# Performance work log

Measured on AMD Instinct MI355X. Metric: run time of the kernel, lower is better.

Reference implementation:

```python
import jax, jax.numpy as jnp
import numpy as np
from jax import lax

B, T, N = 512, 512, 64  # batch, max_seq_len, num_tags


def setup_inputs() -> dict:
    key = jax.random.key(0)
    k1, k2, k3, k4 = jax.random.split(key, 4)
    inputs = jax.random.normal(k1, (B, T, N), dtype=jnp.float32)
    transition_params = jax.random.normal(k2, (N, N), dtype=jnp.float32)
    tag_indices = jax.random.randint(k3, (B, T), 0, N, dtype=jnp.int32)
    sequence_lengths = jax.random.randint(k4, (B,), 0, T, dtype=jnp.int32)
    return {
        "inputs": inputs,
        "transition_params": transition_params,
        "tag_indices": tag_indices,
        "sequence_lengths": sequence_lengths,
    }


def _crf_log_norm(inputs, transition_params, sequence_lengths):
    # inputs: [B, T, N]
    first = inputs[:, 0, :]                       # alpha after first token, [B, N]
    rest = jnp.transpose(inputs[:, 1:, :], (1, 0, 2))  # [T-1, B, N]

    def step(alpha, emit):
        # alpha: [B, N] -> broadcast-add transitions [N, N], logsumexp over prev tag
        new = emit + jax.nn.logsumexp(alpha[:, :, None] + transition_params[None], axis=1)
        return new, new

    _, alphas = lax.scan(step, first, rest)       # [T-1, B, N]
    all_alphas = jnp.concatenate([first[None], alphas], axis=0)  # [T, B, N]
    all_alphas = jnp.transpose(all_alphas, (1, 0, 2))            # [B, T, N]
    last_index = jnp.maximum(0, sequence_lengths - 1)            # [B]
    alpha_last = jnp.take_along_axis(all_alphas, last_index[:, None, None], axis=1)[:, 0, :]
    return jax.nn.logsumexp(alpha_last, axis=1)   # [B]


def _crf_sequence_score(inputs, tag_indices, sequence_lengths, transition_params):
    mask = (jnp.arange(T)[None, :] < sequence_lengths[:, None]).astype(inputs.dtype)  # [B, T]
    # unary: gather emission score of the gold tag at each position
    unary = jnp.take_along_axis(inputs, tag_indices[:, :, None], axis=2)[:, :, 0]      # [B, T]
    unary_scores = jnp.sum(unary * mask, axis=1)
    # binary: transition scores between consecutive gold tags
    binary = transition_params[tag_indices[:, :-1], tag_indices[:, 1:]]                # [B, T-1]
    binary_scores = jnp.sum(binary * mask[:, 1:], axis=1)
    return unary_scores + binary_scores


def reference(inputs, transition_params, tag_indices, sequence_lengths):
    tag_indices = tag_indices.astype(jnp.int32)
    sequence_lengths = sequence_lengths.astype(jnp.int32)
    sequence_scores = _crf_sequence_score(inputs, tag_indices, sequence_lengths, transition_params)
    log_norm = _crf_log_norm(inputs, transition_params, sequence_lengths)
    log_likelihood = sequence_scores - log_norm   # [B]
    return (log_likelihood, transition_params)
```

## Files before the change

kernel.cpp:

```cpp
#include <hip/hip_runtime.h>

#define BB 512
#define TT 512
#define NN 64

__device__ __forceinline__ float readlane_f(float v, int lane) {
    return __int_as_float(__builtin_amdgcn_readlane(__float_as_int(v), lane));
}


#define DOTG(g, Ev) \
    s0 = fmaf(readlane_f(p, 4 * (g) + 0), Ev.x, s0); \
    s1 = fmaf(readlane_f(p, 4 * (g) + 1), Ev.y, s1); \
    s2 = fmaf(readlane_f(p, 4 * (g) + 2), Ev.z, s2); \
    s3 = fmaf(readlane_f(p, 4 * (g) + 3), Ev.w, s3);

#define DOT64(p, sres) { \
    float s0 = readlane_f(p, 0) * E0.x; \
    float s1 = readlane_f(p, 1) * E0.y; \
    float s2 = readlane_f(p, 2) * E0.z; \
    float s3 = readlane_f(p, 3) * E0.w; \
    DOTG(1, E1)  DOTG(2, E2)  DOTG(3, E3) \
    DOTG(4, E4)  DOTG(5, E5)  DOTG(6, E6)  DOTG(7, E7) \
    DOTG(8, E8)  DOTG(9, E9)  DOTG(10, E10) DOTG(11, E11) \
    DOTG(12, E12) DOTG(13, E13) DOTG(14, E14) DOTG(15, E15) \
    sres = (s0 + s1) + (s2 + s3); \
}

__global__ __launch_bounds__(64, 1) void crf_kernel(
    const float* __restrict__ inputs,
    const float* __restrict__ trans,
    const int*   __restrict__ tags,
    const int*   __restrict__ lens,
    float*       __restrict__ out)
{
    const int b = blockIdx.x;
    const int j = threadIdx.x;

    if (b < 64) out[BB + b * 64 + j] = trans[b * 64 + j];

    const int L    = lens[b];
    const int last = (L - 1) > 0 ? (L - 1) : 0;

    const float* inb  = inputs + (size_t)b * TT * NN;
    const int*   tagb = tags + (size_t)b * TT;

    float sc = 0.f;
    #pragma unroll
    for (int k = 0; k < 8; ++k) {
        const int t  = k * 64 + j;
        const int tg = tagb[t];
        if (t < L) sc += inb[t * NN + tg];
        if (t + 1 < L) sc += trans[tg * NN + tagb[t + 1]];
    }
    #pragma unroll
    for (int x = 32; x >= 1; x >>= 1) sc += __shfl_xor(sc, x, 64);

    float4 E0, E1, E2, E3, E4, E5, E6, E7, E8, E9, E10, E11, E12, E13, E14, E15;
#define LDE(Ev, g) \
    Ev.x = __expf(trans[(4 * (g) + 0) * NN + j]); \
    Ev.y = __expf(trans[(4 * (g) + 1) * NN + j]); \
    Ev.z = __expf(trans[(4 * (g) + 2) * NN + j]); \
    Ev.w = __expf(trans[(4 * (g) + 3) * NN + j]);
    LDE(E0, 0)   LDE(E1, 1)   LDE(E2, 2)   LDE(E3, 3)
    LDE(E4, 4)   LDE(E5, 5)   LDE(E6, 6)   LDE(E7, 7)
    LDE(E8, 8)   LDE(E9, 9)   LDE(E10, 10) LDE(E11, 11)
    LDE(E12, 12) LDE(E13, 13) LDE(E14, 14) LDE(E15, 15)
#undef LDE

    float alpha = inb[j];

    float4 pA0, pA1, pA2, pA3, pB0, pB1, pB2, pB3;

#define LD(vec, comp, tt) { const int tc_ = (tt) <= last ? (tt) : last; \
                            vec.comp = inb[tc_ * NN + j]; }
#define LOADCHUNK(v0, v1, v2, v3, base) \
    LD(v0, x, (base) + 0)  LD(v0, y, (base) + 1)  LD(v0, z, (base) + 2)  LD(v0, w, (base) + 3)  \
    LD(v1, x, (base) + 4)  LD(v1, y, (base) + 5)  LD(v1, z, (base) + 6)  LD(v1, w, (base) + 7)  \
    LD(v2, x, (base) + 8)  LD(v2, y, (base) + 9)  LD(v2, z, (base) + 10) LD(v2, w, (base) + 11) \
    LD(v3, x, (base) + 12) LD(v3, y, (base) + 13) LD(v3, z, (base) + 14) LD(v3, w, (base) + 15)

#define STEP(tc_, EM) { \
    const float m = readlane_f(alpha, 0); \
    const float p = __expf(alpha - m); \
    float s; \
    DOT64(p, s) \
    if ((tc_) <= last) alpha = ((EM) + m) + __logf(s); \
}

    LOADCHUNK(pA0, pA1, pA2, pA3, 1)

    for (int t0 = 1; t0 <= last; t0 += 32) {
        LOADCHUNK(pB0, pB1, pB2, pB3, t0 + 16)
        STEP(t0 + 0,  pA0.x) STEP(t0 + 1,  pA0.y) STEP(t0 + 2,  pA0.z) STEP(t0 + 3,  pA0.w)
        STEP(t0 + 4,  pA1.x) STEP(t0 + 5,  pA1.y) STEP(t0 + 6,  pA1.z) STEP(t0 + 7,  pA1.w)
        STEP(t0 + 8,  pA2.x) STEP(t0 + 9,  pA2.y) STEP(t0 + 10, pA2.z) STEP(t0 + 11, pA2.w)
        STEP(t0 + 12, pA3.x) STEP(t0 + 13, pA3.y) STEP(t0 + 14, pA3.z) STEP(t0 + 15, pA3.w)
        LOADCHUNK(pA0, pA1, pA2, pA3, t0 + 32)
        STEP(t0 + 16, pB0.x) STEP(t0 + 17, pB0.y) STEP(t0 + 18, pB0.z) STEP(t0 + 19, pB0.w)
        STEP(t0 + 20, pB1.x) STEP(t0 + 21, pB1.y) STEP(t0 + 22, pB1.z) STEP(t0 + 23, pB1.w)
        STEP(t0 + 24, pB2.x) STEP(t0 + 25, pB2.y) STEP(t0 + 26, pB2.z) STEP(t0 + 27, pB2.w)
        STEP(t0 + 28, pB3.x) STEP(t0 + 29, pB3.y) STEP(t0 + 30, pB3.z) STEP(t0 + 31, pB3.w)
    }
#undef STEP
#undef LOADCHUNK
#undef LD

    float mm = alpha;
    #pragma unroll
    for (int x = 32; x >= 1; x >>= 1) mm = fmaxf(mm, __shfl_xor(mm, x, 64));
    float e = __expf(alpha - mm);
    #pragma unroll
    for (int x = 32; x >= 1; x >>= 1) e += __shfl_xor(e, x, 64);
    if (j == 0) out[b] = sc - (mm + __logf(e));
}

extern "C" void kernel_launch(void* const* d_in, const int* in_sizes, int n_in,
                              void* d_out, int out_size, void* d_ws, size_t ws_size,
                              hipStream_t stream) {
    const float* inputs = (const float*)d_in[0];
    const float* trans  = (const float*)d_in[1];
    const int*   tags   = (const int*)d_in[2];
    const int*   lens   = (const int*)d_in[3];
    float*       out    = (float*)d_out;

    crf_kernel<<<dim3(BB), dim3(64), 0, stream>>>(inputs, trans, tags, lens, out);
}
```

Baseline: 226.6 us.

## Interleave two batch recurrences per wavefront to overlap serial CRF step latency

Each wavefront now runs the forward recurrence for two batch elements (b and b+256) in lockstep, with half as many blocks launched. The goal is to hide the latency of the serial chain in each step (readlane, exp, 64-term dot, log) by giving the scheduler two independent chains to overlap. The max used for stabilisation is now read from the previous alpha instead of the current one, which takes the readlane off the critical path but loosens the guard against exp overflow. The transition exponentials are pinned in registers and the prefetch chunk shrinks to 4 steps per sequence; each pair now runs until the longer of its two sequences is done.

```diff
diff --git a/kernel.cpp b/kernel.cpp
--- a/kernel.cpp
+++ b/kernel.cpp
@@ -3,6 +3,7 @@
 #define BB 512
 #define TT 512
 #define NN 64
+#define NPAIR 256
 
 __device__ __forceinline__ float readlane_f(float v, int lane) {
     return __int_as_float(__builtin_amdgcn_readlane(__float_as_int(v), lane));
@@ -20,12 +21,25 @@
     float s1 = readlane_f(p, 1) * E0.y; \
     float s2 = readlane_f(p, 2) * E0.z; \
     float s3 = readlane_f(p, 3) * E0.w; \
-    DOTG(1, E1)  DOTG(2, E2)  DOTG(3, E3) \
-    DOTG(4, E4)  DOTG(5, E5)  DOTG(6, E6)  DOTG(7, E7) \
-    DOTG(8, E8)  DOTG(9, E9)  DOTG(10, E10) DOTG(11, E11) \
+    DOTG(1, E1)   DOTG(2, E2)   DOTG(3, E3) \
+    DOTG(4, E4)   DOTG(5, E5)   DOTG(6, E6)   DOTG(7, E7) \
+    DOTG(8, E8)   DOTG(9, E9)   DOTG(10, E10) DOTG(11, E11) \
     DOTG(12, E12) DOTG(13, E13) DOTG(14, E14) DOTG(15, E15) \
     sres = (s0 + s1) + (s2 + s3); \
 }
+
+#define STEP1(av, mv, EMv, tc_, lastv) { \
+    const float mu = mv; \
+    const float p  = __expf(av - mu); \
+    mv = readlane_f(av, 0);    \
+    float s; \
+    DOT64(p, s) \
+    if ((tc_) <= lastv) av = ((EMv) + mu) + __logf(s); \
+}
+
+#define DSTEP(r, EA, EB) \
+    STEP1(alpha0, m0, EA, t0 + (r), last0) \
+    STEP1(alpha1, m1, EB, t0 + (r), last1)
 
 __global__ __launch_bounds__(64, 1) void crf_kernel(
     const float* __restrict__ inputs,
@@ -39,22 +53,32 @@
 
     if (b < 64) out[BB + b * 64 + j] = trans[b * 64 + j];
 
-    const int L    = lens[b];
-    const int last = (L - 1) > 0 ? (L - 1) : 0;
+    const int L0 = lens[b];
+    const int L1 = lens[b + NPAIR];
+    const int last0 = (L0 - 1) > 0 ? (L0 - 1) : 0;
+    const int last1 = (L1 - 1) > 0 ? (L1 - 1) : 0;
+    const int lastmax = last0 > last1 ? last0 : last1;
 
-    const float* inb  = inputs + (size_t)b * TT * NN;
-    const int*   tagb = tags + (size_t)b * TT;
+    const float* inb0 = inputs + (size_t)b * TT * NN;
+    const float* inb1 = inputs + (size_t)(b + NPAIR) * TT * NN;
+    const int*   tagb0 = tags + (size_t)b * TT;
+    const int*   tagb1 = tags + (size_t)(b + NPAIR) * TT;
 
-    float sc = 0.f;
+    float sc0 = 0.f, sc1 = 0.f;
     #pragma unroll
     for (int k = 0; k < 8; ++k) {
-        const int t  = k * 64 + j;
-        const int tg = tagb[t];
-        if (t < L) sc += inb[t * NN + tg];
-        if (t + 1 < L) sc += trans[tg * NN + tagb[t + 1]];
+        const int t = k * 64 + j;
+        const int tg0 = tagb0[t];
+        const int tg1 = tagb1[t];
+        if (t < L0) sc0 += inb0[t * NN + tg0];
+        if (t + 1 < L0) sc0 += trans[tg0 * NN + tagb0[t + 1]];
+        if (t < L1) sc1 += inb1[t * NN + tg1];
+        if (t + 1 < L1) sc1 += trans[tg1 * NN + tagb1[t + 1]];
     }
     #pragma unroll
-    for (int x = 32; x >= 1; x >>= 1) sc += __shfl_xor(sc, x, 64);
+    for (int x = 32; x >= 1; x >>= 1) sc0 += __shfl_xor(sc0, x, 64);
+    #pragma unroll
+    for (int x = 32; x >= 1; x >>= 1) sc1 += __shfl_xor(sc1, x, 64);
 
     float4 E0, E1, E2, E3, E4, E5, E6, E7, E8, E9, E10, E11, E12, E13, E14, E15;
 #define LDE(Ev, g) \
@@ -67,52 +91,67 @@
     LDE(E8, 8)   LDE(E9, 9)   LDE(E10, 10) LDE(E11, 11)
     LDE(E12, 12) LDE(E13, 13) LDE(E14, 14) LDE(E15, 15)
 #undef LDE
+#define PIN4(Ev) asm volatile("" : "+v"(Ev.x), "+v"(Ev.y), "+v"(Ev.z), "+v"(Ev.w));
+    PIN4(E0)  PIN4(E1)  PIN4(E2)  PIN4(E3)
+    PIN4(E4)  PIN4(E5)  PIN4(E6)  PIN4(E7)
+    PIN4(E8)  PIN4(E9)  PIN4(E10) PIN4(E11)
+    PIN4(E12) PIN4(E13) PIN4(E14) PIN4(E15)
+#undef PIN4
 
-    float alpha = inb[j];
+    float alpha0 = inb0[j];
+    float alpha1 = inb1[j];
+    float m0 = readlane_f(alpha0, 0);
+    float m1 = readlane_f(alpha1, 0);
 
-    float4 pA0, pA1, pA2, pA3, pB0, pB1, pB2, pB3;
+    float4 s0A, s1A, s0B, s1B;
 
-#define LD(vec, comp, tt) { const int tc_ = (tt) <= last ? (tt) : last; \
-                            vec.comp = inb[tc_ * NN + j]; }
-#define LOADCHUNK(v0, v1, v2, v3, base) \
-    LD(v0, x, (base) + 0)  LD(v0, y, (base) + 1)  LD(v0, z, (base) + 2)  LD(v0, w, (base) + 3)  \
-    LD(v1, x, (base) + 4)  LD(v1, y, (base) + 5)  LD(v1, z, (base) + 6)  LD(v1, w, (base) + 7)  \
-    LD(v2, x, (base) + 8)  LD(v2, y, (base) + 9)  LD(v2, z, (base) + 10) LD(v2, w, (base) + 11) \
-    LD(v3, x, (base) + 12) LD(v3, y, (base) + 13) LD(v3, z, (base) + 14) LD(v3, w, (base) + 15)
+#define LD1(vec, comp, tt, inbp, lastv) { \
+    const int tc_ = (tt) <= lastv ? (tt) : lastv; \
+    vec.comp = inbp[tc_ * NN + j]; }
+#define LOADC4(vec, base, inbp, lastv) \
+    LD1(vec, x, (base) + 0, inbp, lastv) \
+    LD1(vec, y, (base) + 1, inbp, lastv) \
+    LD1(vec, z, (base) + 2, inbp, lastv) \
+    LD1(vec, w, (base) + 3, inbp, lastv)
 
-#define STEP(tc_, EM) { \
-    const float m = readlane_f(alpha, 0); \
-    const float p = __expf(alpha - m); \
-    float s; \
-    DOT64(p, s) \
-    if ((tc_) <= last) alpha = ((EM) + m) + __logf(s); \
-}
+    LOADC4(s0A, 1, inb0, last0)
+    LOADC4(s1A, 1, inb1, last1)
 
-    LOADCHUNK(pA0, pA1, pA2, pA3, 1)
+    for (int t0 = 1; t0 <= lastmax; t0 += 8) {
+        LOADC4(s0B, t0 + 4, inb0, last0)
+        LOADC4(s1B, t0 + 4, inb1, last1)
+        DSTEP(0, s0A.x, s1A.x)
+        DSTEP(1, s0A.y, s1A.y)
+        DSTEP(2, s0A.z, s1A.z)
+        DSTEP(3, s0A.w, s1A.w)
+        LOADC4(s0A, t0 + 8, inb0, last0)
+        LOADC4(s1A, t0 + 8, inb1, last1)
+        DSTEP(4, s0B.x, s1B.x)
+        DSTEP(5, s0B.y, s1B.y)
+        DSTEP(6, s0B.z, s1B.z)
+        DSTEP(7, s0B.w, s1B.w)
+    }
+#undef LOADC4
+#undef LD1
 
-    for (int t0 = 1; t0 <= last; t0 += 32) {
-        LOADCHUNK(pB0, pB1, pB2, pB3, t0 + 16)
-        STEP(t0 + 0,  pA0.x) STEP(t0 + 1,  pA0.y) STEP(t0 + 2,  pA0.z) STEP(t0 + 3,  pA0.w)
-        STEP(t0 + 4,  pA1.x) STEP(t0 + 5,  pA1.y) STEP(t0 + 6,  pA1.z) STEP(t0 + 7,  pA1.w)
-        STEP(t0 + 8,  pA2.x) STEP(t0 + 9,  pA2.y) STEP(t0 + 10, pA2.z) STEP(t0 + 11, pA2.w)
-        STEP(t0 + 12, pA3.x) STEP(t0 + 13, pA3.y) STEP(t0 + 14, pA3.z) STEP(t0 + 15, pA3.w)
-        LOADCHUNK(pA0, pA1, pA2, pA3, t0 + 32)
-        STEP(t0 + 16, pB0.x) STEP(t0 + 17, pB0.y) STEP(t0 + 18, pB0.z) STEP(t0 + 19, pB0.w)
-        STEP(t0 + 20, pB1.x) STEP(t0 + 21, pB1.y) STEP(t0 + 22, pB1.z) STEP(t0 + 23, pB1.w)
-        STEP(t0 + 24, pB2.x) STEP(t0 + 25, pB2.y) STEP(t0 + 26, pB2.z) STEP(t0 + 27, pB2.w)
-        STEP(t0 + 28, pB3.x) STEP(t0 + 29, pB3.y) STEP(t0 + 30, pB3.z) STEP(t0 + 31, pB3.w)
+    {
+        float mm = alpha0;
+        #pragma unroll
+        for (int x = 32; x >= 1; x >>= 1) mm = fmaxf(mm, __shfl_xor(mm, x, 64));
+        float e = __expf(alpha0 - mm);
+        #pragma unroll
+        for (int x = 32; x >= 1; x >>= 1) e += __shfl_xor(e, x, 64);
+        if (j == 0) out[b] = sc0 - (mm + __logf(e));
     }
-#undef STEP
-#undef LOADCHUNK
-#undef LD
-
-    float mm = alpha;
-    #pragma unroll
-    for (int x = 32; x >= 1; x >>= 1) mm = fmaxf(mm, __shfl_xor(mm, x, 64));
-    float e = __expf(alpha - mm);
-    #pragma unroll
-    for (int x = 32; x >= 1; x >>= 1) e += __shfl_xor(e, x, 64);
-    if (j == 0) out[b] = sc - (mm + __logf(e));
+    {
+        float mm = alpha1;
+        #pragma unroll
+        for (int x = 32; x >= 1; x >>= 1) mm = fmaxf(mm, __shfl_xor(mm, x, 64));
+        float e = __expf(alpha1 - mm);
+        #pragma unroll
+        for (int x = 32; x >= 1; x >>= 1) e += __shfl_xor(e, x, 64);
+        if (j == 0) out[b + NPAIR] = sc1 - (mm + __logf(e));
+    }
 }
 
 extern "C" void kernel_launch(void* const* d_in, const int* in_sizes, int n_in,
@@ -124,5 +163,5 @@
     const int*   lens   = (const int*)d_in[3];
     float*       out    = (float*)d_out;
 
-    crf_kernel<<<dim3(BB), dim3(64), 0, stream>>>(inputs, trans, tags, lens, out);
+    crf_kernel<<<dim3(NPAIR), dim3(64), 0, stream>>>(inputs, trans, tags, lens, out);
 }
```

Measured after the change: 348.1 us. 53.6% more time.
